# Kernel tuning notes

Hardware: AMD Instinct MI355X
Metric: run time of the kernel (lower is better)

The kernel has to match this reference:

```python
import jax, jax.numpy as jnp
import numpy as np

B, C, Dd, Hh, Ww = 2, 512, 8, 8, 16
D_STATE, D_CONV, EXPAND = 16, 4, 2
D_INNER = EXPAND * C
DT_RANK = -(-C // 16)  # ceil(C/16), Mamba default dt_rank


def setup_inputs() -> dict:
    key = jax.random.key(0)
    ks = jax.random.split(key, 8)
    s = 0.02
    return {
        "x": jax.random.normal(ks[0], (B, C, Dd, Hh, Ww), jnp.float32),
        "gamma": jnp.ones((C,), jnp.float32),
        "beta": jnp.zeros((C,), jnp.float32),
        "W_in": jax.random.normal(ks[1], (C, 2 * D_INNER), jnp.float32) * s,
        "conv_w": jax.random.normal(ks[2], (D_INNER, D_CONV), jnp.float32) * s,
        "conv_b": jnp.zeros((D_INNER,), jnp.float32),
        "W_x": jax.random.normal(ks[3], (D_INNER, DT_RANK + 2 * D_STATE), jnp.float32) * s,
        "W_dt": jax.random.normal(ks[4], (DT_RANK, D_INNER), jnp.float32) * s,
        "b_dt": jax.random.normal(ks[5], (D_INNER,), jnp.float32) * s,
        "A_log": jnp.log(jnp.broadcast_to(jnp.arange(1, D_STATE + 1, dtype=jnp.float32), (D_INNER, D_STATE))),
        "D_param": jnp.ones((D_INNER,), jnp.float32),
        "W_out": jax.random.normal(ks[6], (D_INNER, C), jnp.float32) * s,
    }


def reference(x, gamma, beta, W_in, conv_w, conv_b, W_x, W_dt, b_dt, A_log, D_param, W_out):
    b, c, d, h, w = x.shape
    L = d * h * w
    dt_rank = W_dt.shape[0]
    n = A_log.shape[1]
    kc = conv_w.shape[1]

    # (B,C,D,H,W) -> (B,L,C)
    xs = x.transpose(0, 2, 3, 4, 1).reshape(b, L, c)

    # LayerNorm over channels
    mu = xs.mean(-1, keepdims=True)
    var = ((xs - mu) ** 2).mean(-1, keepdims=True)
    xn = (xs - mu) * jax.lax.rsqrt(var + 1e-5) * gamma + beta

    # Mamba: in_proj -> (x, z)
    xz = xn @ W_in                       # (b,L,2*di)
    xi, z = jnp.split(xz, 2, axis=-1)

    # causal depthwise conv1d (kernel kc) + SiLU
    xp = jnp.pad(xi, ((0, 0), (kc - 1, 0), (0, 0)))
    xc = conv_b + sum(conv_w[:, k] * xp[:, k:k + L, :] for k in range(kc))
    xc = jax.nn.silu(xc)                 # (b,L,di)

    # x_proj -> dt, B, C (input-dependent)
    proj = xc @ W_x
    dtr = proj[..., :dt_rank]
    Bm = proj[..., dt_rank:dt_rank + n]   # (b,L,n)
    Cm = proj[..., dt_rank + n:]          # (b,L,n)
    dt = jax.nn.softplus(dtr @ W_dt + b_dt)  # (b,L,di)

    A = -jnp.exp(A_log)                  # (di,n)
    dA = jnp.exp(dt[..., None] * A)      # (b,L,di,n)
    dBx = (dt * xc)[..., None] * Bm[:, :, None, :]  # (b,L,di,n)

    def step(hc, inp):
        dA_t, dBx_t, C_t = inp
        hc = dA_t * hc + dBx_t
        return hc, jnp.einsum('bdn,bn->bd', hc, C_t)

    h0 = jnp.zeros((b, dA.shape[2], n), xc.dtype)
    _, ys = jax.lax.scan(step, h0, (dA.transpose(1, 0, 2, 3), dBx.transpose(1, 0, 2, 3), Cm.transpose(1, 0, 2)))
    y = ys.transpose(1, 0, 2) + D_param * xc   # (b,L,di)
    y = y * jax.nn.silu(z)

    out = y @ W_out                      # (b,L,c)
    out = out.reshape(b, d, h, w, c).transpose(0, 4, 1, 2, 3)
    return out + x
```

## Files before the change

### kernel.cpp

```cpp
#include <hip/hip_runtime.h>
#include <hip/hip_bf16.h>


typedef __attribute__((ext_vector_type(8))) short bf16x8;
typedef __attribute__((ext_vector_type(4))) float f32x4;

#define DEV __device__ __forceinline__

DEV short f2bf(float f) {
    union { float f; unsigned u; } v;
    v.f = f;
    unsigned r = v.u + 0x7fffu + ((v.u >> 16) & 1u);
    return (short)(r >> 16);
}
DEV float bf2f(short s) {
    union { float f; unsigned u; } v;
    v.u = ((unsigned)(unsigned short)s) << 16;
    return v.f;
}

__global__ void k_prep(const float* __restrict__ x, const float* __restrict__ Win,
                       const float* __restrict__ Wx, const float* __restrict__ Wdt,
                       const float* __restrict__ Wout, const float* __restrict__ Alog,
                       short* __restrict__ WinT, short* __restrict__ WxT,
                       short* __restrict__ WdtT, short* __restrict__ WoutT,
                       float* __restrict__ xT, float* __restrict__ Aneg) {
    __shared__ float T[64][65];
    int bx = blockIdx.x, tid = threadIdx.x;
    int ii = tid >> 6, jj = tid & 63;

    if (bx < 256) {
        int b = bx >> 7, rem = bx & 127, ct = rem >> 4, lt = rem & 15;
        int c0 = ct * 64, l0 = lt * 64;
        #pragma unroll
        for (int k = 0; k < 16; k++) {
            int c = ii * 16 + k;
            T[c][jj] = x[(b * 512 + c0 + c) * 1024 + l0 + jj];
        }
        __syncthreads();
        #pragma unroll
        for (int k = 0; k < 16; k++) {
            int l = ii * 16 + k;
            xT[(b * 1024 + l0 + l) * 512 + c0 + jj] = T[jj][l];
        }
        return;
    }

    auto xpose = [&](const float* src, short* dst, int R, int C, int rt, int ct) {
        int r0 = rt * 64, c0 = ct * 64;
        #pragma unroll
        for (int k = 0; k < 16; k++) {
            int r = ii * 16 + k;
            if (r0 + r < R) T[r][jj] = src[(size_t)(r0 + r) * C + c0 + jj];
        }
        __syncthreads();
        #pragma unroll
        for (int k = 0; k < 16; k++) {
            int c = ii * 16 + k;
            if (r0 + jj < R) dst[(size_t)(c0 + c) * R + r0 + jj] = f2bf(T[jj][c]);
        }
    };

    if (bx < 512)      { int i = bx - 256; xpose(Win,  WinT,  512, 2048, i >> 5, i & 31); }
    else if (bx < 640) { int i = bx - 512; xpose(Wout, WoutT, 1024, 512, i >> 3, i & 7); }
    else if (bx < 656) { int i = bx - 640; xpose(Wx,   WxT,  1024,  64, i, 0); }
    else if (bx < 672) { int i = bx - 656; xpose(Wdt,  WdtT,   32, 1024, 0, i); }
    else {
        int base = ((bx - 672) * 256 + tid) * 16;
        #pragma unroll
        for (int t = 0; t < 16; t++) Aneg[base + t] = -__expf(Alog[base + t]);
    }
}

__global__ void k_ln(const float* __restrict__ xT, const float* __restrict__ gamma,
                     const float* __restrict__ beta, short* __restrict__ xn) {
    int tid = threadIdx.x;
    int m = blockIdx.x * 8 + (tid >> 5);
    int c0 = (tid & 31) * 16;
    float vx[16], vg[16], vb[16];
    #pragma unroll
    for (int s = 0; s < 4; s++) {
        *(float4*)&vx[s * 4] = *(const float4*)&xT[m * 512 + c0 + s * 4];
        *(float4*)&vg[s * 4] = *(const float4*)&gamma[c0 + s * 4];
        *(float4*)&vb[s * 4] = *(const float4*)&beta[c0 + s * 4];
    }
    float ps = 0.f, pq = 0.f;
    #pragma unroll
    for (int j = 0; j < 16; j++) { ps += vx[j]; pq += vx[j] * vx[j]; }
    #pragma unroll
    for (int off = 1; off < 32; off <<= 1) {
        ps += __shfl_xor(ps, off);
        pq += __shfl_xor(pq, off);
    }
    float mu = ps * (1.f / 512.f);
    float rstd = rsqrtf(pq * (1.f / 512.f) - mu * mu + 1e-5f);
    short t16[16];
    #pragma unroll
    for (int j = 0; j < 16; j++)
        t16[j] = f2bf((vx[j] - mu) * rstd * vg[j] + vb[j]);
    *(uint4*)&xn[m * 512 + c0]     = *(uint4*)&t16[0];
    *(uint4*)&xn[m * 512 + c0 + 8] = *(uint4*)&t16[8];
}

__launch_bounds__(256)
__global__ void k_gemm1(const short* __restrict__ xn, const short* __restrict__ WinT,
                        short* __restrict__ xz) {
    constexpr int LDT = 40;
    __shared__ __align__(16) short As[128 * LDT];
    __shared__ __align__(16) short Bs[128 * LDT];
    int tid = threadIdx.x, lane = tid & 63, wave = tid >> 6;
    int quad = lane >> 4, r16 = lane & 15;
    int wmi = wave >> 1, wni = wave & 1;
    int blockM = blockIdx.y * 128, blockN = blockIdx.x * 128;
    f32x4 acc[4][4] = {};

    for (int k0 = 0; k0 < 512; k0 += 32) {
        #pragma unroll
        for (int idx = tid; idx < 512; idx += 256) {
            int row = idx >> 2, seg = idx & 3;
            *(uint4*)&As[row * LDT + seg * 8] =
                *(const uint4*)&xn[(blockM + row) * 512 + k0 + seg * 8];
        }
        #pragma unroll
        for (int idx = tid; idx < 512; idx += 256) {
            int row = idx >> 2, seg = idx & 3;
            *(uint4*)&Bs[row * LDT + seg * 8] =
                *(const uint4*)&WinT[(blockN + row) * 512 + k0 + seg * 8];
        }
        __syncthreads();
        bf16x8 af[4], bf8[4];
        #pragma unroll
        for (int i = 0; i < 4; i++)
            af[i] = *(const bf16x8*)&As[(wmi * 64 + i * 16 + r16) * LDT + quad * 8];
        #pragma unroll
        for (int j = 0; j < 4; j++)
            bf8[j] = *(const bf16x8*)&Bs[(wni * 64 + j * 16 + r16) * LDT + quad * 8];
        #pragma unroll
        for (int i = 0; i < 4; i++)
            #pragma unroll
            for (int j = 0; j < 4; j++)
                acc[i][j] = __builtin_amdgcn_mfma_f32_16x16x32_bf16(af[i], bf8[j], acc[i][j], 0, 0, 0);
        __syncthreads();
    }
    #pragma unroll
    for (int i = 0; i < 4; i++)
        #pragma unroll
        for (int j = 0; j < 4; j++)
            #pragma unroll
            for (int rr = 0; rr < 4; rr++) {
                int row = blockM + wmi * 64 + i * 16 + quad * 4 + rr;
                int col = blockN + wni * 64 + j * 16 + r16;
                xz[row * 2048 + col] = f2bf(acc[i][j][rr]);
            }
}

__global__ void k_conv_silu(const short* __restrict__ xz, const float* __restrict__ convw,
                            const float* __restrict__ convb, short* __restrict__ xcb) {
    int m = blockIdx.x;
    int b = m >> 10, l = m & 1023;
    for (int d = threadIdx.x; d < 1024; d += 256) {
        float acc = convb[d];
        #pragma unroll
        for (int k = 0; k < 4; k++) {
            int lm = l - 3 + k;
            if (lm >= 0)
                acc += convw[d * 4 + k] * bf2f(xz[(b * 1024 + lm) * 2048 + d]);
        }
        xcb[m * 1024 + d] = f2bf(acc / (1.f + __expf(-acc)));
    }
}

__launch_bounds__(256)
__global__ void k_gemm2s(const short* __restrict__ xcb, const short* __restrict__ WxT,
                         float* __restrict__ projP) {
    constexpr int LDT = 40;
    __shared__ __align__(16) short As[64 * LDT];
    __shared__ __align__(16) short Bs[64 * LDT];
    int tid = threadIdx.x, lane = tid & 63, wave = tid >> 6;
    int quad = lane >> 4, r16 = lane & 15;
    int blockM = blockIdx.y * 64;
    int kc = blockIdx.x;
    int k0base = kc * 128;
    f32x4 acc[4] = {};
    #pragma unroll
    for (int kk = 0; kk < 128; kk += 32) {
        int k0 = k0base + kk;
        { int row = tid >> 2, seg = tid & 3;
          *(uint4*)&As[row * LDT + seg * 8] = *(const uint4*)&xcb[(blockM + row) * 1024 + k0 + seg * 8];
          *(uint4*)&Bs[row * LDT + seg * 8] = *(const uint4*)&WxT[row * 1024 + k0 + seg * 8]; }
        __syncthreads();
        bf16x8 af = *(const bf16x8*)&As[(wave * 16 + r16) * LDT + quad * 8];
        #pragma unroll
        for (int j = 0; j < 4; j++) {
            bf16x8 b8 = *(const bf16x8*)&Bs[(j * 16 + r16) * LDT + quad * 8];
            acc[j] = __builtin_amdgcn_mfma_f32_16x16x32_bf16(af, b8, acc[j], 0, 0, 0);
        }
        __syncthreads();
    }
    float* dst = projP + (size_t)kc * 131072;
    #pragma unroll
    for (int j = 0; j < 4; j++)
        #pragma unroll
        for (int rr = 0; rr < 4; rr++) {
            int row = wave * 16 + quad * 4 + rr;
            int col = j * 16 + r16;
            dst[(blockM + row) * 64 + col] = acc[j][rr];
        }
}

__launch_bounds__(256)
__global__ void k_gemm3(const float* __restrict__ projP, const short* __restrict__ WdtT,
                        const float* __restrict__ bdt, float* __restrict__ proj,
                        short* __restrict__ dth) {
    constexpr int LDT = 40;
    __shared__ __align__(16) char SMB[17408];
    short* As = (short*)SMB;
    short* Bs = (short*)(SMB + 5120);
    short* Dt = (short*)SMB;
    int tid = threadIdx.x, lane = tid & 63, wave = tid >> 6;
    int quad = lane >> 4, r16 = lane & 15;
    int wmi = wave >> 1, wni = wave & 1;
    int blockM = blockIdx.y * 64, blockN = blockIdx.x * 128;

    {
        int row = tid >> 2, seg = tid & 3;
        float s[8] = {};
        #pragma unroll
        for (int kc = 0; kc < 8; kc++) {
            const float* p = projP + (size_t)kc * 131072 + (blockM + row) * 64 + seg * 8;
            float4 a = *(const float4*)p, b = *(const float4*)(p + 4);
            s[0] += a.x; s[1] += a.y; s[2] += a.z; s[3] += a.w;
            s[4] += b.x; s[5] += b.y; s[6] += b.z; s[7] += b.w;
        }
        short t8[8];
        #pragma unroll
        for (int j = 0; j < 8; j++) t8[j] = f2bf(s[j]);
        *(uint4*)&As[row * LDT + seg * 8] = *(uint4*)t8;
    }
    #pragma unroll
    for (int idx = tid; idx < 512; idx += 256) {
        int row = idx >> 2, seg = idx & 3;
        *(uint4*)&Bs[row * LDT + seg * 8] = *(const uint4*)&WdtT[(blockN + row) * 32 + seg * 8];
    }
    if (blockIdx.x == 0) {
        int row = tid >> 2, seg = tid & 3;
        float s[8] = {};
        #pragma unroll
        for (int kc = 0; kc < 8; kc++) {
            const float* p = projP + (size_t)kc * 131072 + (blockM + row) * 64 + 32 + seg * 8;
            float4 a = *(const float4*)p, b = *(const float4*)(p + 4);
            s[0] += a.x; s[1] += a.y; s[2] += a.z; s[3] += a.w;
            s[4] += b.x; s[5] += b.y; s[6] += b.z; s[7] += b.w;
        }
        float* q = &proj[(blockM + row) * 64 + 32 + seg * 8];
        *(float4*)q = make_float4(s[0], s[1], s[2], s[3]);
        *(float4*)(q + 4) = make_float4(s[4], s[5], s[6], s[7]);
    }
    __syncthreads();

    bf16x8 af[2], b8[4];
    #pragma unroll
    for (int i = 0; i < 2; i++)
        af[i] = *(const bf16x8*)&As[(wmi * 32 + i * 16 + r16) * LDT + quad * 8];
    #pragma unroll
    for (int j = 0; j < 4; j++)
        b8[j] = *(const bf16x8*)&Bs[(wni * 64 + j * 16 + r16) * LDT + quad * 8];
    __syncthreads();

    #pragma unroll
    for (int i = 0; i < 2; i++)
        #pragma unroll
        for (int j = 0; j < 4; j++) {
            f32x4 c2 = {};
            c2 = __builtin_amdgcn_mfma_f32_16x16x32_bf16(af[i], b8[j], c2, 0, 0, 0);
            #pragma unroll
            for (int rr = 0; rr < 4; rr++) {
                int row = wmi * 32 + i * 16 + quad * 4 + rr;
                int col = wni * 64 + j * 16 + r16;
                float t = c2[rr] + bdt[blockN + col];
                float sp = (t > 20.f) ? t : __logf(1.f + __expf(t));
                Dt[row * 136 + col] = f2bf(sp);
            }
        }
    __syncthreads();
    {
        int row = tid >> 2, seg = tid & 3;
        #pragma unroll
        for (int u = 0; u < 4; u++)
            *(uint4*)&dth[(blockM + row) * 1024 + blockN + seg * 32 + u * 8] =
                *(uint4*)&Dt[row * 136 + seg * 32 + u * 8];
    }
}

__global__ void k_scanA(const short* __restrict__ dth, const short* __restrict__ xcb,
                        const float* __restrict__ proj, const float* __restrict__ Aneg,
                        float* __restrict__ segP, float* __restrict__ segQ) {
    int bx = blockIdx.x;
    int b = bx >> 7, rem = bx & 127;
    int seg = rem >> 2, dch = rem & 3;
    int tid = threadIdx.x;
    int d = dch * 256 + tid;
    int l0 = seg * 32;
    __shared__ float Bsh[32][16];
    for (int idx = tid; idx < 512; idx += 256) {
        int i = idx >> 4, n = idx & 15;
        Bsh[i][n] = proj[(b * 1024 + l0 + i) * 64 + 32 + n];
    }
    __syncthreads();
    float An[16], P[16], Q[16];
    #pragma unroll
    for (int n = 0; n < 16; n++) { An[n] = Aneg[d * 16 + n]; P[n] = 1.f; Q[n] = 0.f; }
    for (int i = 0; i < 32; i++) {
        int l = l0 + i;
        float dt = bf2f(dth[(b * 1024 + l) * 1024 + d]);
        float xc = bf2f(xcb[(b * 1024 + l) * 1024 + d]);
        float dx = dt * xc;
        #pragma unroll
        for (int n = 0; n < 16; n++) {
            float a = __expf(An[n] * dt);
            P[n] *= a;
            Q[n] = a * Q[n] + dx * Bsh[i][n];
        }
    }
    int base = ((b * 32 + seg) * 1024 + d) * 16;
    #pragma unroll
    for (int n = 0; n < 16; n++) { segP[base + n] = P[n]; segQ[base + n] = Q[n]; }
}

__global__ void k_scanB(float* __restrict__ segP, const float* __restrict__ segQ) {
    int gid = blockIdx.x * 256 + threadIdx.x;
    int b = gid >> 14, r = gid & 16383;
    float h = 0.f;
    for (int seg = 0; seg < 32; seg++) {
        int idx = (b * 32 + seg) * 16384 + r;
        float P = segP[idx], Q = segQ[idx];
        segP[idx] = h;
        h = P * h + Q;
    }
}

__global__ void k_scanC(const short* __restrict__ dth, const short* __restrict__ xcb,
                        const float* __restrict__ proj, const float* __restrict__ Aneg,
                        const float* __restrict__ segH, const short* __restrict__ xz,
                        const float* __restrict__ Dp, short* __restrict__ ybuf) {
    int bx = blockIdx.x;
    int b = bx >> 7, rem = bx & 127;
    int seg = rem >> 2, dch = rem & 3;
    int tid = threadIdx.x;
    int d = dch * 256 + tid;
    int l0 = seg * 32;
    __shared__ float Bsh[32][16], Csh[32][16];
    for (int idx = tid; idx < 512; idx += 256) {
        int i = idx >> 4, n = idx & 15;
        Bsh[i][n] = proj[(b * 1024 + l0 + i) * 64 + 32 + n];
        Csh[i][n] = proj[(b * 1024 + l0 + i) * 64 + 48 + n];
    }
    __syncthreads();
    float An[16], h[16];
    int hbase = ((b * 32 + seg) * 1024 + d) * 16;
    #pragma unroll
    for (int n = 0; n < 16; n++) { An[n] = Aneg[d * 16 + n]; h[n] = segH[hbase + n]; }
    float Dpd = Dp[d];
    for (int i = 0; i < 32; i++) {
        int l = l0 + i;
        float dt = bf2f(dth[(b * 1024 + l) * 1024 + d]);
        float xc = bf2f(xcb[(b * 1024 + l) * 1024 + d]);
        float dx = dt * xc;
        float y = 0.f;
        #pragma unroll
        for (int n = 0; n < 16; n++) {
            float a = __expf(An[n] * dt);
            h[n] = a * h[n] + dx * Bsh[i][n];
            y += h[n] * Csh[i][n];
        }
        float z = bf2f(xz[(b * 1024 + l) * 2048 + 1024 + d]);
        float sz = z / (1.f + __expf(-z));
        ybuf[(b * 1024 + l) * 1024 + d] = f2bf((y + Dpd * xc) * sz);
    }
}

__launch_bounds__(256)
__global__ void k_gemm4(const short* __restrict__ ybuf, const short* __restrict__ WoutT,
                        const float* __restrict__ x, float* __restrict__ out) {
    constexpr int LDT2 = 72;
    __shared__ __align__(16) char SMB[18432];
    short* As = (short*)SMB;
    short* Bs = (short*)(SMB + 9216);
    float (*T)[65] = (float(*)[65])SMB;
    int tid = threadIdx.x, lane = tid & 63, wave = tid >> 6;
    int quad = lane >> 4, r16 = lane & 15;
    int wmi = wave >> 1, wni = wave & 1;
    int blockM = blockIdx.y * 64, blockN = blockIdx.x * 64;
    f32x4 acc[2][2] = {};

    for (int k0 = 0; k0 < 1024; k0 += 64) {
        #pragma unroll
        for (int t = tid; t < 512; t += 256) {
            int row = t >> 3, seg = t & 7;
            *(uint4*)&As[row * LDT2 + seg * 8] = *(const uint4*)&ybuf[(blockM + row) * 1024 + k0 + seg * 8];
            *(uint4*)&Bs[row * LDT2 + seg * 8] = *(const uint4*)&WoutT[(blockN + row) * 1024 + k0 + seg * 8];
        }
        __syncthreads();
        #pragma unroll
        for (int ks = 0; ks < 2; ks++) {
            bf16x8 af[2], b8[2];
            #pragma unroll
            for (int i = 0; i < 2; i++)
                af[i] = *(const bf16x8*)&As[(wmi * 32 + i * 16 + r16) * LDT2 + ks * 32 + quad * 8];
            #pragma unroll
            for (int j = 0; j < 2; j++)
                b8[j] = *(const bf16x8*)&Bs[(wni * 32 + j * 16 + r16) * LDT2 + ks * 32 + quad * 8];
            #pragma unroll
            for (int i = 0; i < 2; i++)
                #pragma unroll
                for (int j = 0; j < 2; j++)
                    acc[i][j] = __builtin_amdgcn_mfma_f32_16x16x32_bf16(af[i], b8[j], acc[i][j], 0, 0, 0);
        }
        __syncthreads();
    }
    #pragma unroll
    for (int i = 0; i < 2; i++)
        #pragma unroll
        for (int j = 0; j < 2; j++)
            #pragma unroll
            for (int rr = 0; rr < 4; rr++)
                T[wmi * 32 + i * 16 + quad * 4 + rr][wni * 32 + j * 16 + r16] = acc[i][j][rr];
    __syncthreads();
    int b = blockM >> 10, l0 = blockM & 1023;
    int ii = tid >> 6, jj = tid & 63;
    #pragma unroll
    for (int k = 0; k < 16; k++) {
        int c = ii * 16 + k;
        int gi = (b * 512 + blockN + c) * 1024 + l0 + jj;
        out[gi] = T[jj][c] + x[gi];
    }
}

extern "C" void kernel_launch(void* const* d_in, const int* in_sizes, int n_in,
                              void* d_out, int out_size, void* d_ws, size_t ws_size,
                              hipStream_t stream) {
    const float* x    = (const float*)d_in[0];
    const float* gam  = (const float*)d_in[1];
    const float* bet  = (const float*)d_in[2];
    const float* Win  = (const float*)d_in[3];
    const float* cw   = (const float*)d_in[4];
    const float* cb   = (const float*)d_in[5];
    const float* Wx   = (const float*)d_in[6];
    const float* Wdt  = (const float*)d_in[7];
    const float* bdt  = (const float*)d_in[8];
    const float* Alog = (const float*)d_in[9];
    const float* Dp   = (const float*)d_in[10];
    const float* Wout = (const float*)d_in[11];
    float* out = (float*)d_out;

    char* w = (char*)d_ws;
    size_t o = 0;
    auto alloc = [&](size_t bytes) { size_t r = o; o += (bytes + 255) & ~255ULL; return r; };

    float* projP = (float*)(w + alloc((size_t)8 * 131072 * 4));
    float* proj  = (float*)(w + alloc(131072 * 4));
    short* WinT  = (short*)(w + alloc(1048576 * 2));
    short* WxT   = (short*)(w + alloc(65536 * 2));
    short* WdtT  = (short*)(w + alloc(32768 * 2));
    short* WoutT = (short*)(w + alloc(524288 * 2));
    float* xT    = (float*)(w + alloc(1048576 * 4));
    short* xn    = (short*)(w + alloc(1048576 * 2));
    float* Aneg  = (float*)(w + alloc(16384 * 4));
    short* xz    = (short*)(w + alloc((size_t)4194304 * 2));
    short* xcb   = (short*)(w + alloc(2097152 * 2));
    short* dth   = (short*)(w + alloc(2097152 * 2));
    float* segP  = (float*)(w + alloc((size_t)1048576 * 4));
    float* segQ  = (float*)(w + alloc((size_t)1048576 * 4));
    short* ybuf  = (short*)(w + alloc(2097152 * 2));
    (void)ws_size; (void)in_sizes; (void)n_in; (void)out_size;

    k_prep<<<676, 256, 0, stream>>>(x, Win, Wx, Wdt, Wout, Alog,
                                    WinT, WxT, WdtT, WoutT, xT, Aneg);
    k_ln<<<256, 256, 0, stream>>>(xT, gam, bet, xn);
    k_gemm1<<<dim3(16, 16), 256, 0, stream>>>(xn, WinT, xz);
    k_conv_silu<<<2048, 256, 0, stream>>>(xz, cw, cb, xcb);
    k_gemm2s<<<dim3(8, 32), 256, 0, stream>>>(xcb, WxT, projP);
    k_gemm3<<<dim3(8, 32), 256, 0, stream>>>(projP, WdtT, bdt, proj, dth);
    k_scanA<<<256, 256, 0, stream>>>(dth, xcb, proj, Aneg, segP, segQ);
    k_scanB<<<128, 256, 0, stream>>>(segP, segQ);
    k_scanC<<<256, 256, 0, stream>>>(dth, xcb, proj, Aneg, segP, xz, Dp, ybuf);
    k_gemm4<<<dim3(8, 32), 256, 0, stream>>>(ybuf, WoutT, x, out);
}
```

Measured before the change: 200.0 us.

## Fuse projection and scan kernels with software grid barriers

Merges the x_proj split-K GEMM with the dt projection GEMM into one persistent kernel, and merges the three scan phases into one kernel. Inside each fused kernel, a global atomic-counter barrier replaces the kernel boundary. This removes three kernel launches and the gaps between them, and it keeps the scan's An registers and shared B/C tiles loaded across phases. In exchange, correctness depends on all 256 blocks being co-resident, since the spin barrier deadlocks otherwise. The scan's middle phase also now uses only half the threads per block.

```diff
diff --git a/kernel.cpp b/kernel.cpp
--- a/kernel.cpp
+++ b/kernel.cpp
@@ -17,6 +17,18 @@
     union { float f; unsigned u; } v;
     v.u = ((unsigned)(unsigned short)s) << 16;
     return v.f;
+}
+
+DEV void gbarrier(unsigned* cnt) {
+    __threadfence();
+    __syncthreads();
+    if (threadIdx.x == 0) {
+        atomicAdd(cnt, 1u);
+        while (__hip_atomic_load(cnt, __ATOMIC_RELAXED, __HIP_MEMORY_SCOPE_AGENT) < 256u)
+            __builtin_amdgcn_s_sleep(2);
+    }
+    __syncthreads();
+    __threadfence();
 }
 
 __global__ void k_prep(const float* __restrict__ x, const float* __restrict__ Win,
@@ -171,178 +183,135 @@
 }
 
 __launch_bounds__(256)
-__global__ void k_gemm2s(const short* __restrict__ xcb, const short* __restrict__ WxT,
-                         float* __restrict__ projP) {
+__global__ void k_proj(const short* __restrict__ xcb, const short* __restrict__ WxT,
+                       const short* __restrict__ WdtT, const float* __restrict__ bdt,
+                       float* __restrict__ projP, float* __restrict__ proj,
+                       short* __restrict__ dth, unsigned* __restrict__ bar) {
     constexpr int LDT = 40;
-    __shared__ __align__(16) short As[64 * LDT];
-    __shared__ __align__(16) short Bs[64 * LDT];
+    __shared__ __align__(16) char SMB[17408];
     int tid = threadIdx.x, lane = tid & 63, wave = tid >> 6;
     int quad = lane >> 4, r16 = lane & 15;
-    int blockM = blockIdx.y * 64;
-    int kc = blockIdx.x;
-    int k0base = kc * 128;
-    f32x4 acc[4] = {};
-    #pragma unroll
-    for (int kk = 0; kk < 128; kk += 32) {
-        int k0 = k0base + kk;
-        { int row = tid >> 2, seg = tid & 3;
-          *(uint4*)&As[row * LDT + seg * 8] = *(const uint4*)&xcb[(blockM + row) * 1024 + k0 + seg * 8];
-          *(uint4*)&Bs[row * LDT + seg * 8] = *(const uint4*)&WxT[row * 1024 + k0 + seg * 8]; }
-        __syncthreads();
-        bf16x8 af = *(const bf16x8*)&As[(wave * 16 + r16) * LDT + quad * 8];
-        #pragma unroll
-        for (int j = 0; j < 4; j++) {
-            bf16x8 b8 = *(const bf16x8*)&Bs[(j * 16 + r16) * LDT + quad * 8];
-            acc[j] = __builtin_amdgcn_mfma_f32_16x16x32_bf16(af, b8, acc[j], 0, 0, 0);
-        }
-        __syncthreads();
-    }
-    float* dst = projP + (size_t)kc * 131072;
-    #pragma unroll
-    for (int j = 0; j < 4; j++)
-        #pragma unroll
-        for (int rr = 0; rr < 4; rr++) {
-            int row = wave * 16 + quad * 4 + rr;
-            int col = j * 16 + r16;
-            dst[(blockM + row) * 64 + col] = acc[j][rr];
-        }
+    int bx = blockIdx.x;
+
+    {
+        short* As = (short*)SMB;
+        short* Bs = (short*)(SMB + 5120);
+        int kc = bx & 7, mt = bx >> 3;
+        int blockM = mt * 64, k0base = kc * 128;
+        f32x4 acc[4] = {};
+        #pragma unroll
+        for (int kk = 0; kk < 128; kk += 32) {
+            int k0 = k0base + kk;
+            { int row = tid >> 2, seg = tid & 3;
+              *(uint4*)&As[row * LDT + seg * 8] = *(const uint4*)&xcb[(blockM + row) * 1024 + k0 + seg * 8];
+              *(uint4*)&Bs[row * LDT + seg * 8] = *(const uint4*)&WxT[row * 1024 + k0 + seg * 8]; }
+            __syncthreads();
+            bf16x8 af = *(const bf16x8*)&As[(wave * 16 + r16) * LDT + quad * 8];
+            #pragma unroll
+            for (int j = 0; j < 4; j++) {
+                bf16x8 b8 = *(const bf16x8*)&Bs[(j * 16 + r16) * LDT + quad * 8];
+                acc[j] = __builtin_amdgcn_mfma_f32_16x16x32_bf16(af, b8, acc[j], 0, 0, 0);
+            }
+            __syncthreads();
+        }
+        float* dst = projP + (size_t)kc * 131072;
+        #pragma unroll
+        for (int j = 0; j < 4; j++)
+            #pragma unroll
+            for (int rr = 0; rr < 4; rr++) {
+                int row = wave * 16 + quad * 4 + rr;
+                int col = j * 16 + r16;
+                dst[(blockM + row) * 64 + col] = acc[j][rr];
+            }
+    }
+
+    gbarrier(bar);
+
+    {
+        short* As = (short*)SMB;
+        short* Bs = (short*)(SMB + 5120);
+        short* Dt = (short*)SMB;
+        int wmi = wave >> 1, wni = wave & 1;
+        int blockM = (bx >> 3) * 64, blockN = (bx & 7) * 128;
+
+        {
+            int row = tid >> 2, seg = tid & 3;
+            float s[8] = {};
+            #pragma unroll
+            for (int kc = 0; kc < 8; kc++) {
+                const float* p = projP + (size_t)kc * 131072 + (blockM + row) * 64 + seg * 8;
+                float4 a = *(const float4*)p, b = *(const float4*)(p + 4);
+                s[0] += a.x; s[1] += a.y; s[2] += a.z; s[3] += a.w;
+                s[4] += b.x; s[5] += b.y; s[6] += b.z; s[7] += b.w;
+            }
+            short t8[8];
+            #pragma unroll
+            for (int j = 0; j < 8; j++) t8[j] = f2bf(s[j]);
+            *(uint4*)&As[row * LDT + seg * 8] = *(uint4*)t8;
+        }
+        #pragma unroll
+        for (int idx = tid; idx < 512; idx += 256) {
+            int row = idx >> 2, seg = idx & 3;
+            *(uint4*)&Bs[row * LDT + seg * 8] = *(const uint4*)&WdtT[(blockN + row) * 32 + seg * 8];
+        }
+        if ((bx & 7) == 0) {
+            int row = tid >> 2, seg = tid & 3;
+            float s[8] = {};
+            #pragma unroll
+            for (int kc = 0; kc < 8; kc++) {
+                const float* p = projP + (size_t)kc * 131072 + (blockM + row) * 64 + 32 + seg * 8;
+                float4 a = *(const float4*)p, b = *(const float4*)(p + 4);
+                s[0] += a.x; s[1] += a.y; s[2] += a.z; s[3] += a.w;
+                s[4] += b.x; s[5] += b.y; s[6] += b.z; s[7] += b.w;
+            }
+            float* q = &proj[(blockM + row) * 64 + 32 + seg * 8];
+            *(float4*)q = make_float4(s[0], s[1], s[2], s[3]);
+            *(float4*)(q + 4) = make_float4(s[4], s[5], s[6], s[7]);
+        }
+        __syncthreads();
+
+        bf16x8 af[2], b8[4];
+        #pragma unroll
+        for (int i = 0; i < 2; i++)
+            af[i] = *(const bf16x8*)&As[(wmi * 32 + i * 16 + r16) * LDT + quad * 8];
+        #pragma unroll
+        for (int j = 0; j < 4; j++)
+            b8[j] = *(const bf16x8*)&Bs[(wni * 64 + j * 16 + r16) * LDT + quad * 8];
+        __syncthreads();
+
+        #pragma unroll
+        for (int i = 0; i < 2; i++)
+            #pragma unroll
+            for (int j = 0; j < 4; j++) {
+                f32x4 c2 = {};
+                c2 = __builtin_amdgcn_mfma_f32_16x16x32_bf16(af[i], b8[j], c2, 0, 0, 0);
+                #pragma unroll
+                for (int rr = 0; rr < 4; rr++) {
+                    int row = wmi * 32 + i * 16 + quad * 4 + rr;
+                    int col = wni * 64 + j * 16 + r16;
+                    float t = c2[rr] + bdt[blockN + col];
+                    float sp = (t > 20.f) ? t : __logf(1.f + __expf(t));
+                    Dt[row * 136 + col] = f2bf(sp);
+                }
+            }
+        __syncthreads();
+        {
+            int row = tid >> 2, seg = tid & 3;
+            #pragma unroll
+            for (int u = 0; u < 4; u++)
+                *(uint4*)&dth[(blockM + row) * 1024 + blockN + seg * 32 + u * 8] =
+                    *(uint4*)&Dt[row * 136 + seg * 32 + u * 8];
+        }
+    }
 }
 
 __launch_bounds__(256)
-__global__ void k_gemm3(const float* __restrict__ projP, const short* __restrict__ WdtT,
-                        const float* __restrict__ bdt, float* __restrict__ proj,
-                        short* __restrict__ dth) {
-    constexpr int LDT = 40;
-    __shared__ __align__(16) char SMB[17408];
-    short* As = (short*)SMB;
-    short* Bs = (short*)(SMB + 5120);
-    short* Dt = (short*)SMB;
-    int tid = threadIdx.x, lane = tid & 63, wave = tid >> 6;
-    int quad = lane >> 4, r16 = lane & 15;
-    int wmi = wave >> 1, wni = wave & 1;
-    int blockM = blockIdx.y * 64, blockN = blockIdx.x * 128;
-
-    {
-        int row = tid >> 2, seg = tid & 3;
-        float s[8] = {};
-        #pragma unroll
-        for (int kc = 0; kc < 8; kc++) {
-            const float* p = projP + (size_t)kc * 131072 + (blockM + row) * 64 + seg * 8;
-            float4 a = *(const float4*)p, b = *(const float4*)(p + 4);
-            s[0] += a.x; s[1] += a.y; s[2] += a.z; s[3] += a.w;
-            s[4] += b.x; s[5] += b.y; s[6] += b.z; s[7] += b.w;
-        }
-        short t8[8];
-        #pragma unroll
-        for (int j = 0; j < 8; j++) t8[j] = f2bf(s[j]);
-        *(uint4*)&As[row * LDT + seg * 8] = *(uint4*)t8;
-    }
-    #pragma unroll
-    for (int idx = tid; idx < 512; idx += 256) {
-        int row = idx >> 2, seg = idx & 3;
-        *(uint4*)&Bs[row * LDT + seg * 8] = *(const uint4*)&WdtT[(blockN + row) * 32 + seg * 8];
-    }
-    if (blockIdx.x == 0) {
-        int row = tid >> 2, seg = tid & 3;
-        float s[8] = {};
-        #pragma unroll
-        for (int kc = 0; kc < 8; kc++) {
-            const float* p = projP + (size_t)kc * 131072 + (blockM + row) * 64 + 32 + seg * 8;
-            float4 a = *(const float4*)p, b = *(const float4*)(p + 4);
-            s[0] += a.x; s[1] += a.y; s[2] += a.z; s[3] += a.w;
-            s[4] += b.x; s[5] += b.y; s[6] += b.z; s[7] += b.w;
-        }
-        float* q = &proj[(blockM + row) * 64 + 32 + seg * 8];
-        *(float4*)q = make_float4(s[0], s[1], s[2], s[3]);
-        *(float4*)(q + 4) = make_float4(s[4], s[5], s[6], s[7]);
-    }
-    __syncthreads();
-
-    bf16x8 af[2], b8[4];
-    #pragma unroll
-    for (int i = 0; i < 2; i++)
-        af[i] = *(const bf16x8*)&As[(wmi * 32 + i * 16 + r16) * LDT + quad * 8];
-    #pragma unroll
-    for (int j = 0; j < 4; j++)
-        b8[j] = *(const bf16x8*)&Bs[(wni * 64 + j * 16 + r16) * LDT + quad * 8];
-    __syncthreads();
-
-    #pragma unroll
-    for (int i = 0; i < 2; i++)
-        #pragma unroll
-        for (int j = 0; j < 4; j++) {
-            f32x4 c2 = {};
-            c2 = __builtin_amdgcn_mfma_f32_16x16x32_bf16(af[i], b8[j], c2, 0, 0, 0);
-            #pragma unroll
-            for (int rr = 0; rr < 4; rr++) {
-                int row = wmi * 32 + i * 16 + quad * 4 + rr;
-                int col = wni * 64 + j * 16 + r16;
-                float t = c2[rr] + bdt[blockN + col];
-                float sp = (t > 20.f) ? t : __logf(1.f + __expf(t));
-                Dt[row * 136 + col] = f2bf(sp);
-            }
-        }
-    __syncthreads();
-    {
-        int row = tid >> 2, seg = tid & 3;
-        #pragma unroll
-        for (int u = 0; u < 4; u++)
-            *(uint4*)&dth[(blockM + row) * 1024 + blockN + seg * 32 + u * 8] =
-                *(uint4*)&Dt[row * 136 + seg * 32 + u * 8];
-    }
-}
-
-__global__ void k_scanA(const short* __restrict__ dth, const short* __restrict__ xcb,
-                        const float* __restrict__ proj, const float* __restrict__ Aneg,
-                        float* __restrict__ segP, float* __restrict__ segQ) {
-    int bx = blockIdx.x;
-    int b = bx >> 7, rem = bx & 127;
-    int seg = rem >> 2, dch = rem & 3;
-    int tid = threadIdx.x;
-    int d = dch * 256 + tid;
-    int l0 = seg * 32;
-    __shared__ float Bsh[32][16];
-    for (int idx = tid; idx < 512; idx += 256) {
-        int i = idx >> 4, n = idx & 15;
-        Bsh[i][n] = proj[(b * 1024 + l0 + i) * 64 + 32 + n];
-    }
-    __syncthreads();
-    float An[16], P[16], Q[16];
-    #pragma unroll
-    for (int n = 0; n < 16; n++) { An[n] = Aneg[d * 16 + n]; P[n] = 1.f; Q[n] = 0.f; }
-    for (int i = 0; i < 32; i++) {
-        int l = l0 + i;
-        float dt = bf2f(dth[(b * 1024 + l) * 1024 + d]);
-        float xc = bf2f(xcb[(b * 1024 + l) * 1024 + d]);
-        float dx = dt * xc;
-        #pragma unroll
-        for (int n = 0; n < 16; n++) {
-            float a = __expf(An[n] * dt);
-            P[n] *= a;
-            Q[n] = a * Q[n] + dx * Bsh[i][n];
-        }
-    }
-    int base = ((b * 32 + seg) * 1024 + d) * 16;
-    #pragma unroll
-    for (int n = 0; n < 16; n++) { segP[base + n] = P[n]; segQ[base + n] = Q[n]; }
-}
-
-__global__ void k_scanB(float* __restrict__ segP, const float* __restrict__ segQ) {
-    int gid = blockIdx.x * 256 + threadIdx.x;
-    int b = gid >> 14, r = gid & 16383;
-    float h = 0.f;
-    for (int seg = 0; seg < 32; seg++) {
-        int idx = (b * 32 + seg) * 16384 + r;
-        float P = segP[idx], Q = segQ[idx];
-        segP[idx] = h;
-        h = P * h + Q;
-    }
-}
-
-__global__ void k_scanC(const short* __restrict__ dth, const short* __restrict__ xcb,
-                        const float* __restrict__ proj, const float* __restrict__ Aneg,
-                        const float* __restrict__ segH, const short* __restrict__ xz,
-                        const float* __restrict__ Dp, short* __restrict__ ybuf) {
+__global__ void k_scan(const short* __restrict__ dth, const short* __restrict__ xcb,
+                       const float* __restrict__ proj, const float* __restrict__ Aneg,
+                       const short* __restrict__ xz, const float* __restrict__ Dp,
+                       float* __restrict__ segP, float* __restrict__ segQ,
+                       short* __restrict__ ybuf, unsigned* __restrict__ bar1,
+                       unsigned* __restrict__ bar2) {
     int bx = blockIdx.x;
     int b = bx >> 7, rem = bx & 127;
     int seg = rem >> 2, dch = rem & 3;
@@ -356,26 +325,69 @@
         Csh[i][n] = proj[(b * 1024 + l0 + i) * 64 + 48 + n];
     }
     __syncthreads();
-    float An[16], h[16];
-    int hbase = ((b * 32 + seg) * 1024 + d) * 16;
-    #pragma unroll
-    for (int n = 0; n < 16; n++) { An[n] = Aneg[d * 16 + n]; h[n] = segH[hbase + n]; }
-    float Dpd = Dp[d];
-    for (int i = 0; i < 32; i++) {
-        int l = l0 + i;
-        float dt = bf2f(dth[(b * 1024 + l) * 1024 + d]);
-        float xc = bf2f(xcb[(b * 1024 + l) * 1024 + d]);
-        float dx = dt * xc;
-        float y = 0.f;
-        #pragma unroll
-        for (int n = 0; n < 16; n++) {
-            float a = __expf(An[n] * dt);
-            h[n] = a * h[n] + dx * Bsh[i][n];
-            y += h[n] * Csh[i][n];
-        }
-        float z = bf2f(xz[(b * 1024 + l) * 2048 + 1024 + d]);
-        float sz = z / (1.f + __expf(-z));
-        ybuf[(b * 1024 + l) * 1024 + d] = f2bf((y + Dpd * xc) * sz);
+    float An[16];
+    #pragma unroll
+    for (int n = 0; n < 16; n++) An[n] = Aneg[d * 16 + n];
+
+    {
+        float P[16], Q[16];
+        #pragma unroll
+        for (int n = 0; n < 16; n++) { P[n] = 1.f; Q[n] = 0.f; }
+        for (int i = 0; i < 32; i++) {
+            int l = l0 + i;
+            float dt = bf2f(dth[(b * 1024 + l) * 1024 + d]);
+            float xc = bf2f(xcb[(b * 1024 + l) * 1024 + d]);
+            float dx = dt * xc;
+            #pragma unroll
+            for (int n = 0; n < 16; n++) {
+                float a = __expf(An[n] * dt);
+                P[n] *= a;
+                Q[n] = a * Q[n] + dx * Bsh[i][n];
+            }
+        }
+        int base = ((b * 32 + seg) * 1024 + d) * 16;
+        #pragma unroll
+        for (int n = 0; n < 16; n++) { segP[base + n] = P[n]; segQ[base + n] = Q[n]; }
+    }
+
+    gbarrier(bar1);
+
+    if (tid < 128) {
+        int gid = bx * 128 + tid;
+        int b2 = gid >> 14, r = gid & 16383;
+        float h = 0.f;
+        for (int s = 0; s < 32; s++) {
+            int idx = (b2 * 32 + s) * 16384 + r;
+            float P = segP[idx], Q = segQ[idx];
+            segP[idx] = h;
+            h = P * h + Q;
+        }
+    }
+
+    gbarrier(bar2);
+
+    {
+        float h[16];
+        int hbase = ((b * 32 + seg) * 1024 + d) * 16;
+        #pragma unroll
+        for (int n = 0; n < 16; n++) h[n] = segP[hbase + n];
+        float Dpd = Dp[d];
+        for (int i = 0; i < 32; i++) {
+            int l = l0 + i;
+            float dt = bf2f(dth[(b * 1024 + l) * 1024 + d]);
+            float xc = bf2f(xcb[(b * 1024 + l) * 1024 + d]);
+            float dx = dt * xc;
+            float y = 0.f;
+            #pragma unroll
+            for (int n = 0; n < 16; n++) {
+                float a = __expf(An[n] * dt);
+                h[n] = a * h[n] + dx * Bsh[i][n];
+                y += h[n] * Csh[i][n];
+            }
+            float z = bf2f(xz[(b * 1024 + l) * 2048 + 1024 + d]);
+            float sz = z / (1.f + __expf(-z));
+            ybuf[(b * 1024 + l) * 1024 + d] = f2bf((y + Dpd * xc) * sz);
+        }
     }
 }
 
@@ -457,6 +469,7 @@
     size_t o = 0;
     auto alloc = [&](size_t bytes) { size_t r = o; o += (bytes + 255) & ~255ULL; return r; };
 
+    unsigned* bars = (unsigned*)(w + alloc(256));
     float* projP = (float*)(w + alloc((size_t)8 * 131072 * 4));
     float* proj  = (float*)(w + alloc(131072 * 4));
     short* WinT  = (short*)(w + alloc(1048576 * 2));
@@ -474,15 +487,14 @@
     short* ybuf  = (short*)(w + alloc(2097152 * 2));
     (void)ws_size; (void)in_sizes; (void)n_in; (void)out_size;
 
+    hipMemsetAsync(bars, 0, 256, stream);
     k_prep<<<676, 256, 0, stream>>>(x, Win, Wx, Wdt, Wout, Alog,
                                     WinT, WxT, WdtT, WoutT, xT, Aneg);
     k_ln<<<256, 256, 0, stream>>>(xT, gam, bet, xn);
     k_gemm1<<<dim3(16, 16), 256, 0, stream>>>(xn, WinT, xz);
     k_conv_silu<<<2048, 256, 0, stream>>>(xz, cw, cb, xcb);
-    k_gemm2s<<<dim3(8, 32), 256, 0, stream>>>(xcb, WxT, projP);
-    k_gemm3<<<dim3(8, 32), 256, 0, stream>>>(projP, WdtT, bdt, proj, dth);
-    k_scanA<<<256, 256, 0, stream>>>(dth, xcb, proj, Aneg, segP, segQ);
-    k_scanB<<<128, 256, 0, stream>>>(segP, segQ);
-    k_scanC<<<256, 256, 0, stream>>>(dth, xcb, proj, Aneg, segP, xz, Dp, ybuf);
+    k_proj<<<256, 256, 0, stream>>>(xcb, WxT, WdtT, bdt, projP, proj, dth, bars);
+    k_scan<<<256, 256, 0, stream>>>(dth, xcb, proj, Aneg, xz, Dp,
+                                    segP, segQ, ybuf, bars + 64, bars + 128);
     k_gemm4<<<dim3(8, 32), 256, 0, stream>>>(ybuf, WoutT, x, out);
 }
```

New measurement: 344.5 us. +72.3%, slower.

## Fuse causal conv+SiLU into x_proj GEMM and widen GEMM blocks to 512 threads

Applied to the files above, without the earlier changes.

The separate conv+SiLU kernel is removed. Its work now happens inside the x_proj GEMM prologue, which computes conv+SiLU into LDS and also writes xcb for the later scan kernels. The conv weights are pre-transposed in the prep kernel so they can be read as vectors. The in_proj and out_proj GEMMs move from 256 to 512 threads per block, giving each wave a smaller tile for more parallelism. This trades fewer registers per wave and extra redundant conv loads for one fewer launch and one less pass over xcb.

```diff
diff --git a/kernel.cpp b/kernel.cpp
--- a/kernel.cpp
+++ b/kernel.cpp
@@ -22,9 +22,11 @@
 __global__ void k_prep(const float* __restrict__ x, const float* __restrict__ Win,
                        const float* __restrict__ Wx, const float* __restrict__ Wdt,
                        const float* __restrict__ Wout, const float* __restrict__ Alog,
+                       const float* __restrict__ convw,
                        short* __restrict__ WinT, short* __restrict__ WxT,
                        short* __restrict__ WdtT, short* __restrict__ WoutT,
-                       float* __restrict__ xT, float* __restrict__ Aneg) {
+                       float* __restrict__ xT, float* __restrict__ Aneg,
+                       float* __restrict__ cwT) {
     __shared__ float T[64][65];
     int bx = blockIdx.x, tid = threadIdx.x;
     int ii = tid >> 6, jj = tid & 63;
@@ -65,10 +67,17 @@
     else if (bx < 640) { int i = bx - 512; xpose(Wout, WoutT, 1024, 512, i >> 3, i & 7); }
     else if (bx < 656) { int i = bx - 640; xpose(Wx,   WxT,  1024,  64, i, 0); }
     else if (bx < 672) { int i = bx - 656; xpose(Wdt,  WdtT,   32, 1024, 0, i); }
-    else {
+    else if (bx < 676) {
         int base = ((bx - 672) * 256 + tid) * 16;
         #pragma unroll
         for (int t = 0; t < 16; t++) Aneg[base + t] = -__expf(Alog[base + t]);
+    } else {
+        #pragma unroll
+        for (int t = 0; t < 16; t++) {
+            int idx = tid * 16 + t;
+            int k = idx >> 10, d = idx & 1023;
+            cwT[idx] = convw[d * 4 + k];
+        }
     }
 }
 
@@ -102,7 +111,7 @@
     *(uint4*)&xn[m * 512 + c0 + 8] = *(uint4*)&t16[8];
 }
 
-__launch_bounds__(256)
+__launch_bounds__(512)
 __global__ void k_gemm1(const short* __restrict__ xn, const short* __restrict__ WinT,
                         short* __restrict__ xz) {
     constexpr int LDT = 40;
@@ -110,92 +119,107 @@
     __shared__ __align__(16) short Bs[128 * LDT];
     int tid = threadIdx.x, lane = tid & 63, wave = tid >> 6;
     int quad = lane >> 4, r16 = lane & 15;
-    int wmi = wave >> 1, wni = wave & 1;
+    int wmi = wave >> 2, wni = wave & 3;
     int blockM = blockIdx.y * 128, blockN = blockIdx.x * 128;
-    f32x4 acc[4][4] = {};
+    f32x4 acc[4][2] = {};
 
     for (int k0 = 0; k0 < 512; k0 += 32) {
-        #pragma unroll
-        for (int idx = tid; idx < 512; idx += 256) {
-            int row = idx >> 2, seg = idx & 3;
+        {
+            int row = tid >> 2, seg = tid & 3;
             *(uint4*)&As[row * LDT + seg * 8] =
                 *(const uint4*)&xn[(blockM + row) * 512 + k0 + seg * 8];
-        }
-        #pragma unroll
-        for (int idx = tid; idx < 512; idx += 256) {
-            int row = idx >> 2, seg = idx & 3;
             *(uint4*)&Bs[row * LDT + seg * 8] =
                 *(const uint4*)&WinT[(blockN + row) * 512 + k0 + seg * 8];
         }
         __syncthreads();
-        bf16x8 af[4], bf8[4];
+        bf16x8 af[4], bf8[2];
         #pragma unroll
         for (int i = 0; i < 4; i++)
             af[i] = *(const bf16x8*)&As[(wmi * 64 + i * 16 + r16) * LDT + quad * 8];
         #pragma unroll
-        for (int j = 0; j < 4; j++)
-            bf8[j] = *(const bf16x8*)&Bs[(wni * 64 + j * 16 + r16) * LDT + quad * 8];
+        for (int j = 0; j < 2; j++)
+            bf8[j] = *(const bf16x8*)&Bs[(wni * 32 + j * 16 + r16) * LDT + quad * 8];
         #pragma unroll
         for (int i = 0; i < 4; i++)
             #pragma unroll
-            for (int j = 0; j < 4; j++)
+            for (int j = 0; j < 2; j++)
                 acc[i][j] = __builtin_amdgcn_mfma_f32_16x16x32_bf16(af[i], bf8[j], acc[i][j], 0, 0, 0);
         __syncthreads();
     }
     #pragma unroll
     for (int i = 0; i < 4; i++)
         #pragma unroll
-        for (int j = 0; j < 4; j++)
+        for (int j = 0; j < 2; j++)
             #pragma unroll
             for (int rr = 0; rr < 4; rr++) {
                 int row = blockM + wmi * 64 + i * 16 + quad * 4 + rr;
-                int col = blockN + wni * 64 + j * 16 + r16;
+                int col = blockN + wni * 32 + j * 16 + r16;
                 xz[row * 2048 + col] = f2bf(acc[i][j][rr]);
             }
 }
 
-__global__ void k_conv_silu(const short* __restrict__ xz, const float* __restrict__ convw,
-                            const float* __restrict__ convb, short* __restrict__ xcb) {
-    int m = blockIdx.x;
-    int b = m >> 10, l = m & 1023;
-    for (int d = threadIdx.x; d < 1024; d += 256) {
-        float acc = convb[d];
-        #pragma unroll
-        for (int k = 0; k < 4; k++) {
-            int lm = l - 3 + k;
-            if (lm >= 0)
-                acc += convw[d * 4 + k] * bf2f(xz[(b * 1024 + lm) * 2048 + d]);
-        }
-        xcb[m * 1024 + d] = f2bf(acc / (1.f + __expf(-acc)));
-    }
-}
-
 __launch_bounds__(256)
-__global__ void k_gemm2s(const short* __restrict__ xcb, const short* __restrict__ WxT,
-                         float* __restrict__ projP) {
-    constexpr int LDT = 40;
+__global__ void k_convgemm2(const short* __restrict__ xz, const float* __restrict__ cwT,
+                            const float* __restrict__ convb, const short* __restrict__ WxT,
+                            short* __restrict__ xcb, float* __restrict__ projP) {
+    constexpr int LDT = 140;
     __shared__ __align__(16) short As[64 * LDT];
     __shared__ __align__(16) short Bs[64 * LDT];
     int tid = threadIdx.x, lane = tid & 63, wave = tid >> 6;
     int quad = lane >> 4, r16 = lane & 15;
-    int blockM = blockIdx.y * 64;
-    int kc = blockIdx.x;
-    int k0base = kc * 128;
+    int kc = blockIdx.x, mt = blockIdx.y;
+    int blockM = mt * 64, d0 = kc * 128;
+
+    #pragma unroll
+    for (int g = 0; g < 4; g++) {
+        int task = tid + 256 * g;
+        int r = task >> 4, u = task & 15;
+        int m = blockM + r, dl = u * 8, d = d0 + dl;
+        float a8[8];
+        {
+            float4 b0 = *(const float4*)&convb[d];
+            float4 b1 = *(const float4*)&convb[d + 4];
+            a8[0] = b0.x; a8[1] = b0.y; a8[2] = b0.z; a8[3] = b0.w;
+            a8[4] = b1.x; a8[5] = b1.y; a8[6] = b1.z; a8[7] = b1.w;
+        }
+        int lrow = m & 1023;
+        #pragma unroll
+        for (int k = 0; k < 4; k++) {
+            if (lrow - 3 + k >= 0) {
+                uint4 raw = *(const uint4*)&xz[(m - 3 + k) * 2048 + d];
+                short* sp = (short*)&raw;
+                float4 w0 = *(const float4*)&cwT[k * 1024 + d];
+                float4 w1 = *(const float4*)&cwT[k * 1024 + d + 4];
+                a8[0] += w0.x * bf2f(sp[0]); a8[1] += w0.y * bf2f(sp[1]);
+                a8[2] += w0.z * bf2f(sp[2]); a8[3] += w0.w * bf2f(sp[3]);
+                a8[4] += w1.x * bf2f(sp[4]); a8[5] += w1.y * bf2f(sp[5]);
+                a8[6] += w1.z * bf2f(sp[6]); a8[7] += w1.w * bf2f(sp[7]);
+            }
+        }
+        short t8[8];
+        #pragma unroll
+        for (int j = 0; j < 8; j++)
+            t8[j] = f2bf(a8[j] / (1.f + __expf(-a8[j])));
+        *(uint4*)&As[r * LDT + dl] = *(uint4*)t8;
+        *(uint4*)&xcb[m * 1024 + d] = *(uint4*)t8;
+    }
+    #pragma unroll
+    for (int g = 0; g < 4; g++) {
+        int task = tid + 256 * g;
+        int n = task >> 4, u = task & 15;
+        *(uint4*)&Bs[n * LDT + u * 8] = *(const uint4*)&WxT[n * 1024 + d0 + u * 8];
+    }
+    __syncthreads();
+
     f32x4 acc[4] = {};
     #pragma unroll
-    for (int kk = 0; kk < 128; kk += 32) {
-        int k0 = k0base + kk;
-        { int row = tid >> 2, seg = tid & 3;
-          *(uint4*)&As[row * LDT + seg * 8] = *(const uint4*)&xcb[(blockM + row) * 1024 + k0 + seg * 8];
-          *(uint4*)&Bs[row * LDT + seg * 8] = *(const uint4*)&WxT[row * 1024 + k0 + seg * 8]; }
-        __syncthreads();
-        bf16x8 af = *(const bf16x8*)&As[(wave * 16 + r16) * LDT + quad * 8];
+    for (int ks = 0; ks < 4; ks++) {
+        bf16x8 af = *(const bf16x8*)&As[(wave * 16 + r16) * LDT + ks * 32 + quad * 8];
         #pragma unroll
         for (int j = 0; j < 4; j++) {
-            bf16x8 b8 = *(const bf16x8*)&Bs[(j * 16 + r16) * LDT + quad * 8];
+            bf16x8 b8 = *(const bf16x8*)&Bs[(j * 16 + r16) * LDT + ks * 32 + quad * 8];
             acc[j] = __builtin_amdgcn_mfma_f32_16x16x32_bf16(af, b8, acc[j], 0, 0, 0);
         }
-        __syncthreads();
     }
     float* dst = projP + (size_t)kc * 131072;
     #pragma unroll
@@ -379,58 +403,51 @@
     }
 }
 
-__launch_bounds__(256)
+__launch_bounds__(512)
 __global__ void k_gemm4(const short* __restrict__ ybuf, const short* __restrict__ WoutT,
                         const float* __restrict__ x, float* __restrict__ out) {
-    constexpr int LDT2 = 72;
-    __shared__ __align__(16) char SMB[18432];
+    constexpr int LDT2 = 76;
+    __shared__ __align__(16) char SMB[19456];
     short* As = (short*)SMB;
-    short* Bs = (short*)(SMB + 9216);
+    short* Bs = (short*)(SMB + 9728);
     float (*T)[65] = (float(*)[65])SMB;
     int tid = threadIdx.x, lane = tid & 63, wave = tid >> 6;
     int quad = lane >> 4, r16 = lane & 15;
-    int wmi = wave >> 1, wni = wave & 1;
+    int wmi = wave >> 2, wni = wave & 3;
     int blockM = blockIdx.y * 64, blockN = blockIdx.x * 64;
-    f32x4 acc[2][2] = {};
+    f32x4 acc[2] = {};
 
     for (int k0 = 0; k0 < 1024; k0 += 64) {
-        #pragma unroll
-        for (int t = tid; t < 512; t += 256) {
-            int row = t >> 3, seg = t & 7;
+        {
+            int row = tid >> 3, seg = tid & 7;
             *(uint4*)&As[row * LDT2 + seg * 8] = *(const uint4*)&ybuf[(blockM + row) * 1024 + k0 + seg * 8];
             *(uint4*)&Bs[row * LDT2 + seg * 8] = *(const uint4*)&WoutT[(blockN + row) * 1024 + k0 + seg * 8];
         }
         __syncthreads();
         #pragma unroll
         for (int ks = 0; ks < 2; ks++) {
-            bf16x8 af[2], b8[2];
+            bf16x8 af[2], b8;
             #pragma unroll
             for (int i = 0; i < 2; i++)
                 af[i] = *(const bf16x8*)&As[(wmi * 32 + i * 16 + r16) * LDT2 + ks * 32 + quad * 8];
-            #pragma unroll
-            for (int j = 0; j < 2; j++)
-                b8[j] = *(const bf16x8*)&Bs[(wni * 32 + j * 16 + r16) * LDT2 + ks * 32 + quad * 8];
+            b8 = *(const bf16x8*)&Bs[(wni * 16 + r16) * LDT2 + ks * 32 + quad * 8];
             #pragma unroll
             for (int i = 0; i < 2; i++)
-                #pragma unroll
-                for (int j = 0; j < 2; j++)
-                    acc[i][j] = __builtin_amdgcn_mfma_f32_16x16x32_bf16(af[i], b8[j], acc[i][j], 0, 0, 0);
+                acc[i] = __builtin_amdgcn_mfma_f32_16x16x32_bf16(af[i], b8, acc[i], 0, 0, 0);
         }
         __syncthreads();
     }
     #pragma unroll
     for (int i = 0; i < 2; i++)
         #pragma unroll
-        for (int j = 0; j < 2; j++)
-            #pragma unroll
-            for (int rr = 0; rr < 4; rr++)
-                T[wmi * 32 + i * 16 + quad * 4 + rr][wni * 32 + j * 16 + r16] = acc[i][j][rr];
+        for (int rr = 0; rr < 4; rr++)
+            T[wmi * 32 + i * 16 + quad * 4 + rr][wni * 16 + r16] = acc[i][rr];
     __syncthreads();
     int b = blockM >> 10, l0 = blockM & 1023;
     int ii = tid >> 6, jj = tid & 63;
     #pragma unroll
-    for (int k = 0; k < 16; k++) {
-        int c = ii * 16 + k;
+    for (int k = 0; k < 8; k++) {
+        int c = ii * 8 + k;
         int gi = (b * 512 + blockN + c) * 1024 + l0 + jj;
         out[gi] = T[jj][c] + x[gi];
     }
@@ -466,6 +483,7 @@
     float* xT    = (float*)(w + alloc(1048576 * 4));
     short* xn    = (short*)(w + alloc(1048576 * 2));
     float* Aneg  = (float*)(w + alloc(16384 * 4));
+    float* cwT   = (float*)(w + alloc(4096 * 4));
     short* xz    = (short*)(w + alloc((size_t)4194304 * 2));
     short* xcb   = (short*)(w + alloc(2097152 * 2));
     short* dth   = (short*)(w + alloc(2097152 * 2));
@@ -474,15 +492,14 @@
     short* ybuf  = (short*)(w + alloc(2097152 * 2));
     (void)ws_size; (void)in_sizes; (void)n_in; (void)out_size;
 
-    k_prep<<<676, 256, 0, stream>>>(x, Win, Wx, Wdt, Wout, Alog,
-                                    WinT, WxT, WdtT, WoutT, xT, Aneg);
+    k_prep<<<677, 256, 0, stream>>>(x, Win, Wx, Wdt, Wout, Alog, cw,
+                                    WinT, WxT, WdtT, WoutT, xT, Aneg, cwT);
     k_ln<<<256, 256, 0, stream>>>(xT, gam, bet, xn);
-    k_gemm1<<<dim3(16, 16), 256, 0, stream>>>(xn, WinT, xz);
-    k_conv_silu<<<2048, 256, 0, stream>>>(xz, cw, cb, xcb);
-    k_gemm2s<<<dim3(8, 32), 256, 0, stream>>>(xcb, WxT, projP);
+    k_gemm1<<<dim3(16, 16), 512, 0, stream>>>(xn, WinT, xz);
+    k_convgemm2<<<dim3(8, 32), 256, 0, stream>>>(xz, cwT, cb, WxT, xcb, projP);
     k_gemm3<<<dim3(8, 32), 256, 0, stream>>>(projP, WdtT, bdt, proj, dth);
     k_scanA<<<256, 256, 0, stream>>>(dth, xcb, proj, Aneg, segP, segQ);
     k_scanB<<<128, 256, 0, stream>>>(segP, segQ);
     k_scanC<<<256, 256, 0, stream>>>(dth, xcb, proj, Aneg, segP, xz, Dp, ybuf);
-    k_gemm4<<<dim3(8, 32), 256, 0, stream>>>(ybuf, WoutT, x, out);
-}
+    k_gemm4<<<dim3(8, 32), 512, 0, stream>>>(ybuf, WoutT, x, out);
+}
```

After: 199.6 us. Within noise of the previous version (-0.2%).
